# Performance work log

Hardware: AMD Instinct MI355X
Metric: run time of the kernel (lower is better)

Reference implementation:

```python
import jax, jax.numpy as jnp
import numpy as np

E = 1024   # embed_dim
H = 16     # num_heads
D = E // H # head_dim
NP = 2     # n_physics
PH = 16    # physics adapter hidden


def setup_inputs() -> dict:
    key = jax.random.key(0)
    ks = jax.random.split(key, 16)
    B, T = 2, 2048
    s = 0.02
    return {
        "x": jax.random.normal(ks[0], (B, T, E), dtype=jnp.float32),
        "physics_state": jax.random.uniform(ks[1], (B, NP), dtype=jnp.float32),
        "attn_mask": jax.random.randint(ks[2], (B, T), 0, 2).astype(jnp.bool_),
        "Wq": jax.random.normal(ks[3], (E, E), dtype=jnp.float32) * s,
        "bq": jnp.zeros((E,), dtype=jnp.float32),
        "Wk": jax.random.normal(ks[4], (E, E), dtype=jnp.float32) * s,
        "bk": jnp.zeros((E,), dtype=jnp.float32),
        "Wv": jax.random.normal(ks[5], (E, E), dtype=jnp.float32) * s,
        "bv": jnp.zeros((E,), dtype=jnp.float32),
        "Wo": jax.random.normal(ks[6], (E, E), dtype=jnp.float32) * s,
        "bo": jnp.zeros((E,), dtype=jnp.float32),
        "Wp1": jax.random.normal(ks[7], (NP, PH), dtype=jnp.float32) * 0.5,
        "bp1": jnp.zeros((PH,), dtype=jnp.float32),
        "Wp2": jax.random.normal(ks[8], (PH, H), dtype=jnp.float32) * 0.25,
        "bp2": jnp.zeros((H,), dtype=jnp.float32),
    }


def reference(x, physics_state, attn_mask, Wq, bq, Wk, bk, Wv, bv, Wo, bo, Wp1, bp1, Wp2, bp2):
    B, T, _ = x.shape
    scale = 1.0 / np.sqrt(D)
    # projections -> (B, H, T, D)
    q = (x @ Wq + bq).reshape(B, T, H, D).transpose(0, 2, 1, 3)
    k = (x @ Wk + bk).reshape(B, T, H, D).transpose(0, 2, 1, 3)
    v = (x @ Wv + bv).reshape(B, T, H, D).transpose(0, 2, 1, 3)
    # per-head physics bias (B, H) -> (B, H, 1, 1)
    h = jax.nn.gelu(physics_state @ Wp1 + bp1, approximate=False)
    phys_bias = (h @ Wp2 + bp2)[:, :, None, None]
    scores = jnp.einsum("bhqd,bhkd->bhqk", q, k) * scale + phys_bias
    # key padding mask: True = keep
    scores = jnp.where(attn_mask[:, None, None, :], scores, -jnp.inf)
    attn = jax.nn.softmax(scores, axis=-1)
    out = jnp.einsum("bhqk,bhkd->bhqd", attn, v)
    out = out.transpose(0, 2, 1, 3).reshape(B, T, E)
    return out @ Wo + bo
```

## Files before the change

kernel.cpp:

```cpp
#include <hip/hip_runtime.h>
#include <hip/hip_bf16.h>
#include <stdint.h>

#define E_  1024
#define H_  16
#define D_  64
#define T_  2048
#define B_  2

typedef unsigned short u16;
typedef unsigned char u8;
typedef __attribute__((ext_vector_type(8))) __bf16 bf16x8;
typedef __attribute__((ext_vector_type(4))) float f32x4;
typedef __attribute__((ext_vector_type(8))) u16 u16x8;
typedef __attribute__((ext_vector_type(4))) u16 u16x4;
typedef __attribute__((ext_vector_type(2))) uint32_t u32x2;

__device__ __forceinline__ float bf2f(u16 u) {
  union { uint32_t u32; float f; } x; x.u32 = ((uint32_t)u) << 16; return x.f;
}
__device__ __forceinline__ u16 f2bf(float v) {
  union { float f; uint32_t u; } x; x.f = v;
  uint32_t r = x.u + 0x7fffu + ((x.u >> 16) & 1u);
  return (u16)(r >> 16);
}
__device__ __forceinline__ void async16(const void* g, void* l) {
  __builtin_amdgcn_global_load_lds(
      (const __attribute__((address_space(1))) void*)g,
      (__attribute__((address_space(3))) void*)l, 16, 0, 0);
}

__device__ __forceinline__ int detect_f32(const void* src) {
  u16 u = ((const u16*)src)[2 * (threadIdx.x & 63)];
  int e = (u >> 7) & 0xFF;
  int ex = (e != 0 && (e <= 0x40 || e >= 0xC0)) ? 1 : 0;
  return __popcll(__ballot(ex)) > 16;
}

__global__ __launch_bounds__(256) void convf_kernel(const void* __restrict__ src,
                                                    u16* __restrict__ dst, int n) {
  const int f32in = detect_f32(src);
  int i = (blockIdx.x * 256 + threadIdx.x) * 8;
  if (i >= n) return;
  if (f32in) {
    const float* s = (const float*)src;
    u16x8 o;
#pragma unroll
    for (int j = 0; j < 8; ++j) o[j] = f2bf(s[i + j]);
    *(u16x8*)(dst + i) = o;
  } else {
    *(u16x8*)(dst + i) = *(const u16x8*)((const u16*)src + i);
  }
}

__global__ __launch_bounds__(256) void bias4_kernel(
    const void* __restrict__ b0, const void* __restrict__ b1,
    const void* __restrict__ b2, const void* __restrict__ b3,
    u16* __restrict__ dst) {
  const void* src = (blockIdx.x == 0) ? b0 : (blockIdx.x == 1) ? b1
                    : (blockIdx.x == 2) ? b2 : b3;
  const int f32in = detect_f32(src);
  u16* d = dst + blockIdx.x * 2048;
  int t = threadIdx.x;
#pragma unroll
  for (int j = 0; j < 4; ++j) {
    int i = t + j * 256;
    d[i] = f32in ? f2bf(((const float*)src)[i]) : ((const u16*)src)[i];
  }
}

__global__ __launch_bounds__(256) void maskbias_kernel(const void* __restrict__ mp,
                                                       float* __restrict__ mbg) {
  unsigned w0 = ((const unsigned*)mp)[threadIdx.x & 63];
  int isInt = (__ballot(w0 > 1u) == 0ull);
  int i = blockIdx.x * 256 + threadIdx.x;
  int keep = isInt ? (((const int*)mp)[i] != 0) : (((const u8*)mp)[i] != 0);
  mbg[i] = keep ? -5.77078016f : -30000.f;
}

__global__ __launch_bounds__(256) void wtc4_kernel(
    const void* __restrict__ W0, const void* __restrict__ W1,
    const void* __restrict__ W2, const void* __restrict__ W3,
    u16* __restrict__ T0, u16* __restrict__ T1,
    u16* __restrict__ T2, u16* __restrict__ T3) {
  __shared__ __align__(16) u16 tile[64][65];
  const int z = blockIdx.z;
  const void* Wv = (z == 0) ? W0 : (z == 1) ? W1 : (z == 2) ? W2 : W3;
  u16* WT = (z == 0) ? T0 : (z == 1) ? T1 : (z == 2) ? T2 : T3;
  const int f32in = detect_f32(Wv);
  const int bx = blockIdx.x * 64, by = blockIdx.y * 64;
  const int t = threadIdx.x;
#pragma unroll
  for (int p = 0; p < 2; ++p) {
    int row = p * 32 + (t >> 3);
    int ch = t & 7;
    if (f32in) {
      const float* s = (const float*)Wv + (size_t)(by + row) * E_ + bx + ch * 8;
#pragma unroll
      for (int j = 0; j < 8; ++j) tile[row][ch * 8 + j] = f2bf(s[j]);
    } else {
      u16x8 v = *(const u16x8*)((const u16*)Wv + (size_t)(by + row) * E_ + bx + ch * 8);
#pragma unroll
      for (int j = 0; j < 8; ++j) tile[row][ch * 8 + j] = v[j];
    }
  }
  __syncthreads();
#pragma unroll
  for (int p = 0; p < 2; ++p) {
    int orow = p * 32 + (t >> 3);
    int ch = t & 7;
    u16x8 v;
#pragma unroll
    for (int j = 0; j < 8; ++j) v[j] = tile[ch * 8 + j][orow];
    *(u16x8*)(WT + (size_t)(bx + orow) * E_ + by + ch * 8) = v;
  }
}

__global__ __launch_bounds__(256, 2) void gemm_qkv_kernel(
    const u16* __restrict__ A, const u16* __restrict__ BTm,
    const u16* __restrict__ biases, u16* __restrict__ Qb,
    u16* __restrict__ Kb, u16* __restrict__ Vtb) {
  __shared__ __align__(16) u16 As[128 * 64];
  __shared__ __align__(16) u16 Bs[128 * 64];
  const int tid = threadIdx.x, lane = tid & 63, wid = tid >> 6;
  const int wm = wid >> 1, wn = wid & 1;
  const int l15 = lane & 15, lg = lane >> 4;
  const int r0 = blockIdx.x * 128, c0 = blockIdx.y * 128;
  f32x4 acc[4][4] = {};

  for (int k0 = 0; k0 < E_; k0 += 64) {
    __syncthreads();
#pragma unroll
    for (int i = 0; i < 4; ++i) {
      int row = i * 32 + (tid >> 3);
      int g = (tid & 7) ^ (row & 7);
      async16(A + (size_t)(r0 + row) * E_ + k0 + g * 8,
              (char*)As + i * 4096 + tid * 16);
      async16(BTm + (size_t)(c0 + row) * E_ + k0 + g * 8,
              (char*)Bs + i * 4096 + tid * 16);
    }
    __syncthreads();
#pragma unroll
    for (int kk = 0; kk < 2; ++kk) {
      bf16x8 af[4], bfr[4];
#pragma unroll
      for (int mt = 0; mt < 4; ++mt) {
        int rowa = wm * 64 + mt * 16 + l15;
        int sa = (kk * 4 + lg) ^ (rowa & 7);
        af[mt] = *(const bf16x8*)((const char*)As + rowa * 128 + sa * 16);
        int rowb = wn * 64 + mt * 16 + l15;
        int sb = (kk * 4 + lg) ^ (rowb & 7);
        bfr[mt] = *(const bf16x8*)((const char*)Bs + rowb * 128 + sb * 16);
      }
#pragma unroll
      for (int mt = 0; mt < 4; ++mt)
#pragma unroll
        for (int nt = 0; nt < 4; ++nt)
          acc[mt][nt] = __builtin_amdgcn_mfma_f32_16x16x32_bf16(
              af[mt], bfr[nt], acc[mt][nt], 0, 0, 0);
    }
  }

  const int sel = c0 >> 10;
  u16* outp = (sel == 0) ? Qb : Kb;
#pragma unroll
  for (int mt = 0; mt < 4; ++mt) {
#pragma unroll
    for (int nt = 0; nt < 4; ++nt) {
      int colG = c0 + wn * 64 + nt * 16 + l15;
      int colL = colG & 1023;
      float bv = bf2f(biases[sel * 2048 + colL]);
      int rbase = r0 + wm * 64 + mt * 16 + lg * 4;
      int hh = colL >> 6, dd = colL & 63;
      if (sel == 2) {
        int bb = rbase >> 11, t0 = rbase & (T_ - 1);
        u16x4 pk;
#pragma unroll
        for (int r = 0; r < 4; ++r) pk[r] = f2bf(acc[mt][nt][r] + bv);
        *(u16x4*)(Vtb + (size_t)((bb * H_ + hh) * D_ + dd) * T_ + t0) = pk;
      } else {
#pragma unroll
        for (int r = 0; r < 4; ++r) {
          int row = rbase + r;
          int bb = row >> 11, t = row & (T_ - 1);
          outp[(size_t)((bb * H_ + hh) * T_ + t) * D_ + dd] =
              f2bf(acc[mt][nt][r] + bv);
        }
      }
    }
  }
}

__global__ __launch_bounds__(256, 2) void gemm_out_kernel(
    const u16* __restrict__ A, const u16* __restrict__ BTm,
    const u16* __restrict__ bias, float* __restrict__ out) {
  __shared__ __align__(16) u16 As[128 * 64];
  __shared__ __align__(16) u16 Bs[128 * 64];
  const int tid = threadIdx.x, lane = tid & 63, wid = tid >> 6;
  const int wm = wid >> 1, wn = wid & 1;
  const int l15 = lane & 15, lg = lane >> 4;
  const int r0 = blockIdx.x * 128, c0 = blockIdx.y * 128;
  f32x4 acc[4][4] = {};

  for (int k0 = 0; k0 < E_; k0 += 64) {
    __syncthreads();
#pragma unroll
    for (int i = 0; i < 4; ++i) {
      int row = i * 32 + (tid >> 3);
      int g = (tid & 7) ^ (row & 7);
      async16(A + (size_t)(r0 + row) * E_ + k0 + g * 8,
              (char*)As + i * 4096 + tid * 16);
      async16(BTm + (size_t)(c0 + row) * E_ + k0 + g * 8,
              (char*)Bs + i * 4096 + tid * 16);
    }
    __syncthreads();
#pragma unroll
    for (int kk = 0; kk < 2; ++kk) {
      bf16x8 af[4], bfr[4];
#pragma unroll
      for (int mt = 0; mt < 4; ++mt) {
        int rowa = wm * 64 + mt * 16 + l15;
        int sa = (kk * 4 + lg) ^ (rowa & 7);
        af[mt] = *(const bf16x8*)((const char*)As + rowa * 128 + sa * 16);
        int rowb = wn * 64 + mt * 16 + l15;
        int sb = (kk * 4 + lg) ^ (rowb & 7);
        bfr[mt] = *(const bf16x8*)((const char*)Bs + rowb * 128 + sb * 16);
      }
#pragma unroll
      for (int mt = 0; mt < 4; ++mt)
#pragma unroll
        for (int nt = 0; nt < 4; ++nt)
          acc[mt][nt] = __builtin_amdgcn_mfma_f32_16x16x32_bf16(
              af[mt], bfr[nt], acc[mt][nt], 0, 0, 0);
    }
  }

#pragma unroll
  for (int mt = 0; mt < 4; ++mt)
#pragma unroll
    for (int nt = 0; nt < 4; ++nt) {
      int col = c0 + wn * 64 + nt * 16 + l15;
      float bv = bf2f(bias[col]);
      int rbase = r0 + wm * 64 + mt * 16 + lg * 4;
#pragma unroll
      for (int r = 0; r < 4; ++r)
        out[(size_t)(rbase + r) * E_ + col] = acc[mt][nt][r] + bv;
    }
}

__global__ __launch_bounds__(256, 2) void attn_kernel(
    const u16* __restrict__ Q, const u16* __restrict__ K,
    const u16* __restrict__ VT, const float* __restrict__ mbg,
    u16* __restrict__ outb) {
  __shared__ __align__(16) u16 Ks[2][64 * 64];
  __shared__ __align__(16) u16 Vs[2][64 * 64];
  __shared__ __align__(16) u16 Ps[4][2][2][512];
  __shared__ __align__(16) float mb[T_];
  const int wg = blockIdx.x;
  const int xcd = wg & 7, slot = wg >> 3;
  const int bh = xcd + 8 * (slot >> 4);
  const int q0 = (slot & 15) * 128;
  const int b = bh >> 4, h = bh & 15;
  const int tid = threadIdx.x, lane = tid & 63, w = tid >> 6;
  const int l15 = lane & 15, lg = lane >> 4;

  for (int i = tid; i < T_; i += 256) mb[i] = mbg[b * T_ + i];

  const u16* qb = Q + (size_t)bh * T_ * D_;
  const u16* kb = K + (size_t)bh * T_ * D_;
  const u16* vb = VT + (size_t)bh * D_ * T_;

  bf16x8 qf[2][2];
#pragma unroll
  for (int mt = 0; mt < 2; ++mt)
#pragma unroll
    for (int kd = 0; kd < 2; ++kd) {
      int row = q0 + w * 32 + mt * 16 + l15;
      qf[mt][kd] = *(const bf16x8*)(qb + (size_t)row * D_ + kd * 32 + lg * 8);
    }

#define STAGE(kt_, bi_)                                                  \
  do {                                                                   \
    _Pragma("unroll")                                                    \
    for (int c = 0; c < 2; ++c) {                                        \
      int row_ = c * 32 + (tid >> 3);                                    \
      int g_ = (tid & 7) ^ (row_ & 7);                                   \
      async16(kb + (size_t)((kt_) * 64 + row_) * D_ + g_ * 8,            \
              (char*)&Ks[bi_][0] + c * 4096 + tid * 16);                 \
      async16(vb + (size_t)row_ * T_ + (kt_) * 64 + g_ * 8,              \
              (char*)&Vs[bi_][0] + c * 4096 + tid * 16);                 \
    }                                                                    \
  } while (0)

  STAGE(0, 0);
  __syncthreads();

  f32x4 o[2][4] = {};
  float lrow[2] = {0.f, 0.f};
  const float cc = 0.125f * 1.44269504f;

  for (int kt = 0; kt < 32; ++kt) {
    const int cur = kt & 1;
    if (kt < 31) STAGE(kt + 1, cur ^ 1);
    const char* Kc = (const char*)&Ks[cur][0];
    const char* Vc = (const char*)&Vs[cur][0];
    const int kk0 = kt * 64;

    f32x4 s2[2][4] = {};
#pragma unroll
    for (int kd = 0; kd < 2; ++kd) {
      bf16x8 kf[4];
#pragma unroll
      for (int mf = 0; mf < 4; ++mf) {
        int row = mf * 16 + l15;
        int sl = (kd * 4 + lg) ^ (row & 7);
        kf[mf] = *(const bf16x8*)(Kc + row * 128 + sl * 16);
      }
      __builtin_amdgcn_s_setprio(1);
#pragma unroll
      for (int mt = 0; mt < 2; ++mt)
#pragma unroll
        for (int mf = 0; mf < 4; ++mf)
          s2[mt][mf] = __builtin_amdgcn_mfma_f32_16x16x32_bf16(
              kf[mf], qf[mt][kd], s2[mt][mf], 0, 0, 0);
      __builtin_amdgcn_s_setprio(0);
    }

#pragma unroll
    for (int mt = 0; mt < 2; ++mt) {
#pragma unroll
      for (int mf = 0; mf < 4; ++mf) {
        f32x4 mb4 = *(const f32x4*)&mb[kk0 + mf * 16 + lg * 4];
        float p0 = exp2f(fmaf(s2[mt][mf][0], cc, mb4[0]));
        float p1 = exp2f(fmaf(s2[mt][mf][1], cc, mb4[1]));
        float p2 = exp2f(fmaf(s2[mt][mf][2], cc, mb4[2]));
        float p3 = exp2f(fmaf(s2[mt][mf][3], cc, mb4[3]));
        lrow[mt] += (p0 + p1) + (p2 + p3);
        uint32_t w0, w1;
        asm("v_cvt_pk_bf16_f32 %0, %1, %2" : "=v"(w0) : "v"(p0), "v"(p1));
        asm("v_cvt_pk_bf16_f32 %0, %1, %2" : "=v"(w1) : "v"(p2), "v"(p3));
        u32x2 pk = {w0, w1};
        int lgr = (mf & 1) * 2 + (lg >> 1);
        *(u32x2*)((char*)&Ps[w][mt][mf >> 1][0] +
                  (l15 + 16 * lgr) * 16 + 8 * (lg & 1)) = pk;
      }
    }

    asm volatile("s_waitcnt lgkmcnt(0)" ::: "memory");
    __builtin_amdgcn_sched_barrier(0);

#pragma unroll
    for (int kk = 0; kk < 2; ++kk) {
      bf16x8 pf[2], vf[4];
#pragma unroll
      for (int mt = 0; mt < 2; ++mt)
        pf[mt] = *(const bf16x8*)((const char*)&Ps[w][mt][kk][0] + lane * 16);
#pragma unroll
      for (int df = 0; df < 4; ++df) {
        int row = df * 16 + l15;
        int sl = (kk * 4 + lg) ^ (row & 7);
        vf[df] = *(const bf16x8*)(Vc + row * 128 + sl * 16);
      }
      __builtin_amdgcn_s_setprio(1);
#pragma unroll
      for (int mt = 0; mt < 2; ++mt)
#pragma unroll
        for (int df = 0; df < 4; ++df)
          o[mt][df] = __builtin_amdgcn_mfma_f32_16x16x32_bf16(
              pf[mt], vf[df], o[mt][df], 0, 0, 0);
      __builtin_amdgcn_s_setprio(0);
    }
    __syncthreads();
  }
#undef STAGE

  float inv[2][4];
#pragma unroll
  for (int mt = 0; mt < 2; ++mt) {
    float t = lrow[mt];
    t += __shfl_xor(t, 16);
    t += __shfl_xor(t, 32);
    float ti = (t > 0.f) ? 1.0f / t : 0.f;
#pragma unroll
    for (int r = 0; r < 4; ++r)
      inv[mt][r] = __shfl(ti, (lane & 48) | (lg * 4 + r));
  }

  char* wbase = ((w < 2) ? (char*)&Ks[0][0] : (char*)&Vs[0][0]) + (w & 1) * 4608;
#pragma unroll
  for (int mt = 0; mt < 2; ++mt)
#pragma unroll
    for (int df = 0; df < 4; ++df)
#pragma unroll
      for (int r = 0; r < 4; ++r) {
        int prow = mt * 16 + lg * 4 + r;
        *(u16*)(wbase + prow * 144 + (df * 16 + l15) * 2) =
            f2bf(o[mt][df][r] * inv[mt][r]);
      }
  asm volatile("s_waitcnt lgkmcnt(0)" ::: "memory");
  __builtin_amdgcn_sched_barrier(0);
  {
    int rowL = lane >> 1;
    int c8 = lane & 1;
    int grow = b * T_ + q0 + w * 32 + rowL;
#pragma unroll
    for (int j = 0; j < 4; ++j) {
      int chunk = c8 + 2 * j;
      u16x8 v = *(const u16x8*)(wbase + rowL * 144 + chunk * 16);
      *(u16x8*)(outb + (size_t)grow * E_ + h * D_ + chunk * 8) = v;
    }
  }
}

extern "C" void kernel_launch(void* const* d_in, const int* in_sizes, int n_in,
                              void* d_out, int out_size, void* d_ws, size_t ws_size,
                              hipStream_t stream) {
  const void* x    = d_in[0];
  const void* mask = d_in[2];
  const void* Wq = d_in[3];
  const void* bq = d_in[4];
  const void* Wk = d_in[5];
  const void* bk = d_in[6];
  const void* Wv = d_in[7];
  const void* bv = d_in[8];
  const void* Wo = d_in[9];
  const void* bo = d_in[10];
  char* ws = (char*)d_ws;

  const size_t MB = 1024 * 1024;
  u16* Kb   = (u16*)(ws + 0 * MB);
  u16* Vtb  = (u16*)(ws + 8 * MB);
  u16* Ab   = (u16*)(ws + 16 * MB);
  u16* WqT  = (u16*)(ws + 16 * MB);
  u16* WkT  = (u16*)(ws + 18 * MB);
  u16* WvT  = (u16*)(ws + 20 * MB);
  u16* WoT  = (u16*)(ws + 24 * MB);
  u16* bqc  = (u16*)(ws + 26 * MB);
  u16* boc  = bqc + 3 * 2048;
  float* mbg = (float*)(ws + 26 * MB + 32 * 1024);

  u16* Qb = (u16*)d_out;
  u16* xc = (u16*)((char*)d_out + 8 * MB);
  float* out = (float*)d_out;

  dim3 blk(256);
  const int NX = B_ * T_ * E_;

  convf_kernel<<<NX / 8 / 256, blk, 0, stream>>>(x, xc, NX);
  bias4_kernel<<<4, blk, 0, stream>>>(bq, bk, bv, bo, bqc);
  maskbias_kernel<<<16, blk, 0, stream>>>(mask, mbg);
  wtc4_kernel<<<dim3(16, 16, 4), blk, 0, stream>>>(Wq, Wk, Wv, Wo,
                                                   WqT, WkT, WvT, WoT);
  gemm_qkv_kernel<<<dim3(32, 24), blk, 0, stream>>>(xc, WqT, bqc, Qb, Kb, Vtb);
  attn_kernel<<<dim3(512), blk, 0, stream>>>(Qb, Kb, Vtb, mbg, Ab);
  gemm_out_kernel<<<dim3(32, 8), blk, 0, stream>>>(Ab, WoT, boc, out);
}
```

Baseline: 136.4 us.

## Keep softmax probabilities in registers by permuting V^T key order

Permutes the key index within each 64-key block when writing V^T from the QKV projection. Each lane's packed bf16 probabilities from the QK MFMA output can then feed the PV MFMA directly as its A operand, with no round trip through shared memory. This removes the Ps LDS buffer, its writes and reads, and the lgkmcnt wait plus sched barrier. The mask/bias row is now read per tile from global memory instead of being staged into LDS, which cuts LDS use and may raise occupancy but adds global loads in the loop.

```diff
diff --git a/kernel.cpp b/kernel.cpp
--- a/kernel.cpp
+++ b/kernel.cpp
@@ -14,7 +14,6 @@
 typedef __attribute__((ext_vector_type(4))) float f32x4;
 typedef __attribute__((ext_vector_type(8))) u16 u16x8;
 typedef __attribute__((ext_vector_type(4))) u16 u16x4;
-typedef __attribute__((ext_vector_type(2))) uint32_t u32x2;
 
 __device__ __forceinline__ float bf2f(u16 u) {
   union { uint32_t u32; float f; } x; x.u32 = ((uint32_t)u) << 16; return x.f;
@@ -28,6 +27,9 @@
   __builtin_amdgcn_global_load_lds(
       (const __attribute__((address_space(1))) void*)g,
       (__attribute__((address_space(3))) void*)l, 16, 0, 0);
+}
+__device__ __forceinline__ int jperm(int k) {
+  return (k & 35) | ((k & 12) << 1) | ((k & 16) >> 2);
 }
 
 __device__ __forceinline__ int detect_f32(const void* src) {
@@ -174,10 +176,11 @@
       int hh = colL >> 6, dd = colL & 63;
       if (sel == 2) {
         int bb = rbase >> 11, t0 = rbase & (T_ - 1);
+        int tp = (t0 & ~63) | jperm(t0 & 63);
         u16x4 pk;
 #pragma unroll
         for (int r = 0; r < 4; ++r) pk[r] = f2bf(acc[mt][nt][r] + bv);
-        *(u16x4*)(Vtb + (size_t)((bb * H_ + hh) * D_ + dd) * T_ + t0) = pk;
+        *(u16x4*)(Vtb + (size_t)((bb * H_ + hh) * D_ + dd) * T_ + tp) = pk;
       } else {
 #pragma unroll
         for (int r = 0; r < 4; ++r) {
@@ -254,8 +257,6 @@
     u16* __restrict__ outb) {
   __shared__ __align__(16) u16 Ks[2][64 * 64];
   __shared__ __align__(16) u16 Vs[2][64 * 64];
-  __shared__ __align__(16) u16 Ps[4][2][2][512];
-  __shared__ __align__(16) float mb[T_];
   const int wg = blockIdx.x;
   const int xcd = wg & 7, slot = wg >> 3;
   const int bh = xcd + 8 * (slot >> 4);
@@ -264,11 +265,10 @@
   const int tid = threadIdx.x, lane = tid & 63, w = tid >> 6;
   const int l15 = lane & 15, lg = lane >> 4;
 
-  for (int i = tid; i < T_; i += 256) mb[i] = mbg[b * T_ + i];
-
   const u16* qb = Q + (size_t)bh * T_ * D_;
   const u16* kb = K + (size_t)bh * T_ * D_;
   const u16* vb = VT + (size_t)bh * D_ * T_;
+  const float* mbb = mbg + b * T_ + lg * 4;
 
   bf16x8 qf[2][2];
 #pragma unroll
@@ -304,7 +304,11 @@
     if (kt < 31) STAGE(kt + 1, cur ^ 1);
     const char* Kc = (const char*)&Ks[cur][0];
     const char* Vc = (const char*)&Vs[cur][0];
-    const int kk0 = kt * 64;
+
+    f32x4 mbv4[4];
+#pragma unroll
+    for (int mf = 0; mf < 4; ++mf)
+      mbv4[mf] = *(const f32x4*)(mbb + kt * 64 + mf * 16);
 
     f32x4 s2[2][4] = {};
 #pragma unroll
@@ -326,35 +330,33 @@
       __builtin_amdgcn_s_setprio(0);
     }
 
+    uint32_t pkw[2][4][2];
 #pragma unroll
     for (int mt = 0; mt < 2; ++mt) {
 #pragma unroll
       for (int mf = 0; mf < 4; ++mf) {
-        f32x4 mb4 = *(const f32x4*)&mb[kk0 + mf * 16 + lg * 4];
-        float p0 = exp2f(fmaf(s2[mt][mf][0], cc, mb4[0]));
-        float p1 = exp2f(fmaf(s2[mt][mf][1], cc, mb4[1]));
-        float p2 = exp2f(fmaf(s2[mt][mf][2], cc, mb4[2]));
-        float p3 = exp2f(fmaf(s2[mt][mf][3], cc, mb4[3]));
+        float p0 = exp2f(fmaf(s2[mt][mf][0], cc, mbv4[mf][0]));
+        float p1 = exp2f(fmaf(s2[mt][mf][1], cc, mbv4[mf][1]));
+        float p2 = exp2f(fmaf(s2[mt][mf][2], cc, mbv4[mf][2]));
+        float p3 = exp2f(fmaf(s2[mt][mf][3], cc, mbv4[mf][3]));
         lrow[mt] += (p0 + p1) + (p2 + p3);
-        uint32_t w0, w1;
-        asm("v_cvt_pk_bf16_f32 %0, %1, %2" : "=v"(w0) : "v"(p0), "v"(p1));
-        asm("v_cvt_pk_bf16_f32 %0, %1, %2" : "=v"(w1) : "v"(p2), "v"(p3));
-        u32x2 pk = {w0, w1};
-        int lgr = (mf & 1) * 2 + (lg >> 1);
-        *(u32x2*)((char*)&Ps[w][mt][mf >> 1][0] +
-                  (l15 + 16 * lgr) * 16 + 8 * (lg & 1)) = pk;
-      }
-    }
-
-    asm volatile("s_waitcnt lgkmcnt(0)" ::: "memory");
-    __builtin_amdgcn_sched_barrier(0);
+        asm("v_cvt_pk_bf16_f32 %0, %1, %2" : "=v"(pkw[mt][mf][0]) : "v"(p0), "v"(p1));
+        asm("v_cvt_pk_bf16_f32 %0, %1, %2" : "=v"(pkw[mt][mf][1]) : "v"(p2), "v"(p3));
+      }
+    }
 
 #pragma unroll
     for (int kk = 0; kk < 2; ++kk) {
       bf16x8 pf[2], vf[4];
 #pragma unroll
-      for (int mt = 0; mt < 2; ++mt)
-        pf[mt] = *(const bf16x8*)((const char*)&Ps[w][mt][kk][0] + lane * 16);
+      for (int mt = 0; mt < 2; ++mt) {
+        union { uint32_t u[4]; bf16x8 v; } pu;
+        pu.u[0] = pkw[mt][2 * kk][0];
+        pu.u[1] = pkw[mt][2 * kk][1];
+        pu.u[2] = pkw[mt][2 * kk + 1][0];
+        pu.u[3] = pkw[mt][2 * kk + 1][1];
+        pf[mt] = pu.v;
+      }
 #pragma unroll
       for (int df = 0; df < 4; ++df) {
         int row = df * 16 + l15;
```

After: 129.0 us. 1.06x faster.
